# Optimization experiments

Hardware: AMD Instinct MI355X
Metric: run time of the kernel (lower is better)

## Reference

```python
import jax, jax.numpy as jnp
import numpy as np

B, S, F_IN, H, F_OUT, BB = 128, 1024, 128, 256, 128, 256


def setup_inputs() -> dict:
    key = jax.random.key(0)
    ks = jax.random.split(key, 16)
    s_in = 1.0 / np.sqrt(F_IN + H)
    s_bb = 1.0 / np.sqrt(BB)
    s_h = 1.0 / np.sqrt(H)
    return {
        "x": jax.random.normal(ks[0], (B, S, F_IN), dtype=jnp.float32),
        "ts": jax.random.uniform(ks[1], (B, S), dtype=jnp.float32),
        # backbone (depth=1): Linear(F_IN+H -> BB)
        "Wb": jax.random.normal(ks[2], (F_IN + H, BB), dtype=jnp.float32) * s_in,
        "bb": jnp.zeros((BB,), jnp.float32),
        # CfC heads: ff1, ff2, time_a, time_b (BB -> H)
        "Wff1": jax.random.normal(ks[3], (BB, H), dtype=jnp.float32) * s_bb,
        "bff1": jnp.zeros((H,), jnp.float32),
        "Wff2": jax.random.normal(ks[4], (BB, H), dtype=jnp.float32) * s_bb,
        "bff2": jnp.zeros((H,), jnp.float32),
        "Wta": jax.random.normal(ks[5], (BB, H), dtype=jnp.float32) * s_bb,
        "bta": jnp.zeros((H,), jnp.float32),
        "Wtb": jax.random.normal(ks[6], (BB, H), dtype=jnp.float32) * s_bb,
        "btb": jnp.zeros((H,), jnp.float32),
        # output projection Linear(H -> F_OUT)
        "Wout": jax.random.normal(ks[7], (H, F_OUT), dtype=jnp.float32) * s_h,
        "bout": jnp.zeros((F_OUT,), jnp.float32),
    }


def reference(x, ts, Wb, bb, Wff1, bff1, Wff2, bff2, Wta, bta, Wtb, btb, Wout, bout):
    # x: [B,S,F_IN], ts: [B,S] -> out: [B,S,F_OUT]
    batch = x.shape[0]
    hidden = Wff1.shape[1]

    def step(h, inp):
        xt, tt = inp  # xt: [B,F_IN], tt: [B]
        z = jnp.tanh(jnp.concatenate([xt, h], axis=-1) @ Wb + bb)  # backbone [B,BB]
        ff1 = jnp.tanh(z @ Wff1 + bff1)
        ff2 = jnp.tanh(z @ Wff2 + bff2)
        t_a = z @ Wta + bta
        t_b = z @ Wtb + btb
        t_interp = jax.nn.sigmoid(t_a * tt[:, None] + t_b)  # time-dependent gate
        h_new = ff1 * (1.0 - t_interp) + t_interp * ff2
        y = h_new @ Wout + bout
        return h_new, y

    h0 = jnp.zeros((batch, hidden), dtype=x.dtype)
    xs = (jnp.swapaxes(x, 0, 1), jnp.swapaxes(ts, 0, 1))  # time-major for scan
    _, ys = jax.lax.scan(step, h0, xs)  # ys: [S,B,F_OUT]
    return jnp.swapaxes(ys, 0, 1)
```

## Files before the change

kernel.cpp:

```cpp
#include <hip/hip_runtime.h>

#define Bn   128
#define Sn   1024
#define FIN  128
#define Hn   256
#define FOUT 128
#define KBB  384
#define NT1  512

#define NR4 20
#define NL4 1
#define DYN_SMEM ((32 * 256 * 8 + NL4 * 1024 * 8) * 2)

#define NL6 11
#define PF6 12
#define DYN6 ((16 * 256 * 8 + NL6 * 512 * 8) * 2)

#define WB_OFF 0
#define W4_OFF 98304
#define WO_OFF 360448
#define WS_HALVES 393216
#define HBUF_OFF WS_HALVES
#define XC_OFF (HBUF_OFF + (size_t)Bn * Sn * Hn)
#define WS_SPLIT_BYTES ((size_t)(WS_HALVES + (size_t)Bn * Sn * Hn) * 2)
#define WS_FULL_BYTES ((XC_OFF + (size_t)Bn * Sn * Hn) * 2)
#define MBOX_BYTE_OFF WS_FULL_BYTES
#define MBOX_FLOATS ((size_t)Bn * 2 * 2 * 256)
#define CNT_BYTE_OFF (MBOX_BYTE_OFF + MBOX_FLOATS * 4)
#define WS_PAIR_BYTES (CNT_BYTE_OFF + 256 * 4)

typedef _Float16 h2 __attribute__((ext_vector_type(2)));
typedef _Float16 h8 __attribute__((ext_vector_type(8)));

__device__ __forceinline__ float dot2f(h2 a, h2 b, float c) {
#if __has_builtin(__builtin_amdgcn_fdot2)
  return __builtin_amdgcn_fdot2(a, b, c, false);
#else
  return c + (float)a[0] * (float)b[0] + (float)a[1] * (float)b[1];
#endif
}
__device__ __forceinline__ void dot8_4(h8 v, h8 w, float& c0, float& c1, float& c2, float& c3) {
  h2 v0 = {v[0], v[1]}, v1 = {v[2], v[3]}, v2 = {v[4], v[5]}, v3 = {v[6], v[7]};
  h2 w0 = {w[0], w[1]}, w1 = {w[2], w[3]}, w2 = {w[4], w[5]}, w3 = {w[6], w[7]};
  c0 = dot2f(v0, w0, c0); c1 = dot2f(v1, w1, c1);
  c2 = dot2f(v2, w2, c2); c3 = dot2f(v3, w3, c3);
}

__global__ __launch_bounds__(256) void pack_w(
    const float* __restrict__ Wb, const float* __restrict__ W1,
    const float* __restrict__ W2, const float* __restrict__ W3,
    const float* __restrict__ W4, const float* __restrict__ Wo,
    _Float16* __restrict__ ws) {
  int p = blockIdx.x * 256 + threadIdx.x;
  if (p >= WS_HALVES) return;
  float v;
  if (p < W4_OFF) {
    int r = p & 7, j = (p >> 3) & 255;
    int k = ((p >> 11) << 3) | r;
    v = Wb[k * 256 + j];
  } else if (p < WO_OFF) {
    int q = p - W4_OFF;
    int r = q & 7, j = (q >> 3) & 1023;
    int k = ((q >> 13) << 3) | r;
    int jj = j & 255;
    const float* Ws = (j < 256) ? W1 : (j < 512) ? W2 : (j < 768) ? W3 : W4;
    v = Ws[k * 256 + jj];
  } else {
    int q = p - WO_OFF;
    int r = q & 7, j = (q >> 3) & 127;
    int k = ((q >> 10) << 3) | r;
    v = Wo[k * 128 + j];
  }
  ws[p] = (_Float16)v;
}

__global__ void zcnt(unsigned* __restrict__ c) { c[threadIdx.x] = 0; }

__global__ __launch_bounds__(256) void xgemm(
    const float* __restrict__ x, const _Float16* __restrict__ ws,
    _Float16* __restrict__ xc) {
  __shared__ __align__(16) _Float16 sX[64 * 128];
  const int tid = threadIdx.x;
  const size_t r0 = (size_t)blockIdx.x * 64;
  const float* xb = x + r0 * 128;
#pragma unroll
  for (int m = 0; m < 32; ++m)
    sX[m * 256 + tid] = (_Float16)xb[m * 256 + tid];
  const _Float16* gX = ws + WB_OFF + (size_t)tid * 8;
  h8 wx[16];
#pragma unroll
  for (int L = 0; L < 16; ++L) wx[L] = *(const h8*)(gX + (size_t)L * 2048);
  __syncthreads();
  for (int r = 0; r < 64; ++r) {
    float c0 = 0.f, c1 = 0.f, c2 = 0.f, c3 = 0.f;
#pragma unroll
    for (int L = 0; L < 16; ++L) {
      h8 v = *(const h8*)&sX[r * 128 + L * 8];
      dot8_4(v, wx[L], c0, c1, c2, c3);
    }
    xc[(r0 + r) * 256 + tid] = (_Float16)(c0 + c1 + c2 + c3);
  }
}

__global__ __launch_bounds__(NT1) void cfc6(
    const float* __restrict__ ts, const float* __restrict__ bb,
    const float* __restrict__ bf1, const float* __restrict__ bf2,
    const float* __restrict__ bta, const float* __restrict__ btb,
    _Float16* __restrict__ ws, unsigned* __restrict__ cnt,
    float* __restrict__ mbox) {
  __shared__ __align__(16) _Float16 hl[128];
  __shared__ __align__(16) _Float16 zfs[Hn];
  __shared__ float tsb[Sn];
  __shared__ float scrZ[256];
  __shared__ float scrH[384];
  extern __shared__ __align__(16) _Float16 dyn[];
  _Float16* sWbh = dyn;
  _Float16* sW4L = dyn + 16 * 256 * 8;

  const int tid = threadIdx.x;
  const int row = blockIdx.x & 127;
  const int hf  = blockIdx.x >> 7;

  const _Float16* Wb_p = ws + WB_OFF;
  const _Float16* W4_p = ws + W4_OFF;
  _Float16* hbuf = ws + HBUF_OFF;
  const _Float16* xcp = ws + XC_OFF;
  const float* tsrow = ts + (size_t)row * Sn;

  const int jz = tid & 255, kq = tid >> 8;
  const int head = tid >> 7, jj = tid & 127;
  const int jcol = head * 256 + hf * 128 + jj;
  const float bbj = (tid < 256) ? bb[tid] : 0.f;
  const float bH =
      (head == 0 ? bf1 : head == 1 ? bf2 : head == 2 ? bta : btb)[hf * 128 + jj];
  const _Float16* gH = W4_p + (size_t)jcol * 8;

  {
    const h8* src = (const h8*)(Wb_p + (size_t)(16 + hf * 16) * 2048);
    h8* dst = (h8*)sWbh;
    for (int i = tid; i < 16 * 256; i += NT1) dst[i] = src[i];
  }
#pragma unroll
  for (int c = 0; c < NL6; ++c)
    *(h8*)&sW4L[((size_t)c * 512 + tid) * 8] = *(const h8*)(gH + (size_t)c * 8192);
  for (int i = tid; i < Sn; i += NT1) tsb[i] = tsrow[i];
  if (tid < 128) hl[tid] = (_Float16)0.f;

  float* mb_me       = mbox + (size_t)(row * 2 + hf) * 512;
  float* mb_pt       = mbox + (size_t)(row * 2 + (1 - hf)) * 512;
  unsigned* c_me = cnt + row * 2 + hf;
  unsigned* c_pt = cnt + row * 2 + (1 - hf);
  __syncthreads();

  for (unsigned st = 0; st < Sn; ++st) {
    h8 wpf[PF6];
#pragma unroll
    for (int c = 0; c < PF6; ++c)
      wpf[c] = *(const h8*)(gH + (size_t)(NL6 + c) * 8192);
    float xcv = 0.f;
    if (tid < 256) xcv = (float)xcp[((size_t)row * Sn + st) * 256 + tid];

    float a0 = 0.f, a1 = 0.f, a2 = 0.f, a3 = 0.f;
#pragma unroll
    for (int c = kq * 8; c < kq * 8 + 8; ++c) {
      h8 v = *(const h8*)&hl[c * 8];
      h8 w = *(const h8*)&sWbh[((size_t)c * 256 + jz) * 8];
      dot8_4(v, w, a0, a1, a2, a3);
    }
    float zs = a0 + a1 + a2 + a3;
    if (kq) scrZ[jz] = zs;
    __syncthreads();
    float zp = 0.f;
    if (tid < 256) {
      zp = zs + scrZ[tid];
      (void)__hip_atomic_exchange(&mb_me[(st & 1) * 256 + tid], zp,
                                  __ATOMIC_RELAXED, __HIP_MEMORY_SCOPE_AGENT);
    }
    __syncthreads();
    if (tid == 0) {
      __hip_atomic_fetch_add(c_me, 1u, __ATOMIC_RELAXED, __HIP_MEMORY_SCOPE_AGENT);
      while (__hip_atomic_fetch_add(c_pt, 0u, __ATOMIC_RELAXED,
                                    __HIP_MEMORY_SCOPE_AGENT) <= st)
        __builtin_amdgcn_s_sleep(1);
    }
    __syncthreads();
    if (tid < 256) {
      float pz = __hip_atomic_fetch_add(&mb_pt[(st & 1) * 256 + tid], 0.0f,
                                        __ATOMIC_RELAXED, __HIP_MEMORY_SCOPE_AGENT);
      zfs[tid] = (_Float16)tanhf(zp + pz + xcv + bbj);
    }
    __syncthreads();

    float s0 = 0.f, s1 = 0.f, s2 = 0.f, s3 = 0.f;
#pragma unroll 2
    for (int c = NL6 + PF6; c < 32; ++c) {
      h8 v = *(const h8*)&zfs[c * 8];
      h8 w = *(const h8*)(gH + (size_t)c * 8192);
      dot8_4(v, w, s0, s1, s2, s3);
    }
#pragma unroll
    for (int c = 0; c < PF6; ++c) asm volatile("" : "+v"(wpf[c]));
#pragma unroll
    for (int c = 0; c < PF6; ++c) {
      h8 v = *(const h8*)&zfs[(NL6 + c) * 8];
      dot8_4(v, wpf[c], s0, s1, s2, s3);
    }
    float b0 = 0.f, b1 = 0.f, b2 = 0.f, b3 = 0.f;
#pragma unroll
    for (int c = 0; c < NL6; ++c) {
      h8 v = *(const h8*)&zfs[c * 8];
      h8 w = *(const h8*)&sW4L[((size_t)c * 512 + tid) * 8];
      dot8_4(v, w, b0, b1, b2, b3);
    }
    float g = (s0 + b0) + (s1 + b1) + (s2 + b2) + (s3 + b3) + bH;
    if (head) scrH[(head - 1) * 128 + jj] = g;
    __syncthreads();
    if (head == 0) {
      float ff2 = scrH[jj], ta = scrH[128 + jj], tb = scrH[256 + jj];
      float tt = tsb[st];
      float sg = 1.f / (1.f + __expf(-(ta * tt + tb)));
      float hn = tanhf(g) * (1.f - sg) + sg * tanhf(ff2);
      hl[jj] = (_Float16)hn;
      hbuf[((size_t)row * Sn + st) * Hn + hf * 128 + jj] = (_Float16)hn;
    }
    __syncthreads();
  }
}

template <int XC, int INLINE_Y>
__global__ __launch_bounds__(NT1, 2) void cfc5(
    const float* __restrict__ x, const float* __restrict__ ts,
    const float* __restrict__ bb, const float* __restrict__ bf1,
    const float* __restrict__ bf2, const float* __restrict__ bta,
    const float* __restrict__ btb, const float* __restrict__ bo,
    _Float16* __restrict__ ws, float* __restrict__ out) {
  __shared__ __align__(16) _Float16 xh[KBB];
  __shared__ __align__(16) _Float16 zf[Hn];
  __shared__ float tsb[Sn];
  __shared__ float scrZ[256];
  __shared__ float scrH[512];
  extern __shared__ __align__(16) _Float16 dyn[];
  _Float16* sWb  = dyn;
  _Float16* sW4L = dyn + 32 * 256 * 8;

  const int tid = threadIdx.x;
  const int b = blockIdx.x;
  const _Float16* Wb_p = ws + WB_OFF;
  const _Float16* W4_p = ws + W4_OFF;
  const _Float16* Wo_p = ws + WO_OFF;
  _Float16* hbuf = ws + HBUF_OFF;
  const _Float16* xcp = ws + XC_OFF;

  const float* xrow  = x  + (size_t)b * Sn * FIN;
  const float* tsrow = ts + (size_t)b * Sn;
  float*       orow  = out + (size_t)b * Sn * FOUT;

  const int jz = tid & 255, kz = tid >> 8;
  const float bbj = (tid < 256) ? bb[tid] : 0.f;
  const float bHA = (tid < 256) ? bf1[tid] : bf2[tid - 256];
  const float bHB = (tid < 256) ? bta[tid] : btb[tid - 256];
  const int jY = tid & 127, kqY = tid >> 7;
  const float boj = bo[jY];

  if (XC) {
    const h8* src = (const h8*)(Wb_p + (size_t)16 * 2048);
    h8* dst = (h8*)sWb;
    for (int i = tid; i < 8192; i += NT1) dst[i] = src[i];
  }
  {
    const h8* src = (const h8*)(W4_p + (size_t)NR4 * 8192);
    h8* dst = (h8*)sW4L;
    for (int i = tid; i < NL4 * 1024; i += NT1) dst[i] = src[i];
  }
  for (int i = tid; i < Sn; i += NT1) tsb[i] = tsrow[i];
  if (tid < 128) ((unsigned*)xh)[64 + tid] = 0;
  if (!XC && tid < 64) {
    float2 xv = *(const float2*)(xrow + 2 * tid);
    h2 p; p[0] = (_Float16)xv.x; p[1] = (_Float16)xv.y;
    *(h2*)&xh[2 * tid] = p;
  }

  const _Float16* gA = W4_p + (size_t)tid * 8;
  const _Float16* gB = W4_p + (size_t)(tid + 512) * 8;
  h8 wA[NR4], wBv[NR4];
#pragma unroll
  for (int c = 0; c < NR4; ++c) {
    wA[c]  = *(const h8*)(gA + (size_t)c * 8192);
    wBv[c] = *(const h8*)(gB + (size_t)c * 8192);
  }
#pragma unroll
  for (int c = 0; c < NR4; ++c) {
    asm volatile("" : "+v"(wA[c]));
    asm volatile("" : "+v"(wBv[c]));
  }
  __syncthreads();

  for (int st = 0; st < Sn; ++st) {
    float xcv = 0.f;
    if (XC && tid < 256)
      xcv = (float)xcp[((size_t)b * Sn + st) * 256 + tid];
    float2 xv; xv.x = 0.f; xv.y = 0.f;
    if (!XC && tid >= 448 && st + 1 < Sn)
      xv = *(const float2*)(xrow + (size_t)(st + 1) * FIN + 2 * (tid - 448));

    float a0 = 0.f, a1 = 0.f, a2 = 0.f, a3 = 0.f;
    if (XC) {
#pragma unroll 4
      for (int c = 0; c < 16; ++c) {
        int kc = kz * 16 + c;
        h8 v = *(const h8*)&xh[128 + kc * 8];
        h8 w = *(const h8*)&sWb[((size_t)kc * 256 + jz) * 8];
        dot8_4(v, w, a0, a1, a2, a3);
      }
    } else {
      const _Float16* gZ = Wb_p + ((size_t)(kz * 24) * 256 + jz) * 8;
#pragma unroll 4
      for (int c = 0; c < 24; ++c) {
        h8 v = *(const h8*)&xh[(kz * 24 + c) * 8];
        h8 w = *(const h8*)(gZ + (size_t)c * 2048);
        dot8_4(v, w, a0, a1, a2, a3);
      }
    }
    float zs = a0 + a1 + a2 + a3;
    if (kz) scrZ[jz] = zs;
    __syncthreads();
    if (tid < 256) {
      float zp = zs + scrZ[tid] + bbj;
      if (XC) zp += xcv;
      zf[tid] = (_Float16)tanhf(zp);
    }
    if (!XC && tid >= 448 && st + 1 < Sn) {
      h2 p; p[0] = (_Float16)xv.x; p[1] = (_Float16)xv.y;
      *(h2*)&xh[2 * (tid - 448)] = p;
    }
    __syncthreads();

    float hA0 = 0.f, hA1 = 0.f, hA2 = 0.f, hA3 = 0.f;
    float hB0 = 0.f, hB1 = 0.f, hB2 = 0.f, hB3 = 0.f;
#pragma unroll 2
    for (int c = NR4 + NL4; c < 32; ++c) {
      h8 v  = *(const h8*)&zf[c * 8];
      h8 wa = *(const h8*)(gA + (size_t)c * 8192);
      h8 wb = *(const h8*)(gB + (size_t)c * 8192);
      dot8_4(v, wa, hA0, hA1, hA2, hA3);
      dot8_4(v, wb, hB0, hB1, hB2, hB3);
    }
#pragma unroll
    for (int c = 0; c < NR4; ++c) {
      h8 v = *(const h8*)&zf[c * 8];
      dot8_4(v, wA[c],  hA0, hA1, hA2, hA3);
      dot8_4(v, wBv[c], hB0, hB1, hB2, hB3);
    }
#pragma unroll
    for (int l = 0; l < NL4; ++l) {
      h8 v  = *(const h8*)&zf[(NR4 + l) * 8];
      h8 wa = *(const h8*)&sW4L[((size_t)l * 1024 + tid) * 8];
      h8 wb = *(const h8*)&sW4L[((size_t)l * 1024 + tid + 512) * 8];
      dot8_4(v, wa, hA0, hA1, hA2, hA3);
      dot8_4(v, wb, hB0, hB1, hB2, hB3);
    }
    float gAv = hA0 + hA1 + hA2 + hA3 + bHA;
    float gBv = hB0 + hB1 + hB2 + hB3 + bHB;
    if (tid >= 256) {
      scrH[tid - 256]       = gAv;
      scrH[256 + tid - 256] = gBv;
    }
    __syncthreads();
    if (tid < 256) {
      float ff2v = scrH[tid], tbv = scrH[256 + tid];
      float tt = tsb[st];
      float sg = 1.f / (1.f + __expf(-(gBv * tt + tbv)));
      float hn = tanhf(gAv) * (1.f - sg) + sg * tanhf(ff2v);
      xh[128 + tid] = (_Float16)hn;
      if (!INLINE_Y)
        hbuf[((size_t)b * Sn + st) * Hn + tid] = (_Float16)hn;
    }
    __syncthreads();

    if (INLINE_Y) {
      const _Float16* gY = Wo_p + ((size_t)(kqY * 8) * 128 + jY) * 8;
      float y0 = 0.f, y1 = 0.f, y2 = 0.f, y3 = 0.f;
#pragma unroll
      for (int c = 0; c < 8; ++c) {
        h8 v = *(const h8*)&xh[128 + (kqY * 8 + c) * 8];
        h8 w = *(const h8*)(gY + (size_t)c * 1024);
        dot8_4(v, w, y0, y1, y2, y3);
      }
      float ysv = y0 + y1 + y2 + y3;
      if (kqY) scrH[(kqY - 1) * 128 + jY] = ysv;
      __syncthreads();
      if (kqY == 0) {
        float y = ysv + boj + scrH[jY] + scrH[128 + jY] + scrH[256 + jY];
        orow[(size_t)st * FOUT + jY] = y;
      }
    }
  }
}

#define SMEMY (65536 + 4096)
extern "C" __global__ __launch_bounds__(256, 4)
void ygemm(const _Float16* __restrict__ ws, const float* __restrict__ bo,
           float* __restrict__ out) {
  extern __shared__ char ysm[];
  _Float16* sWo = (_Float16*)ysm;
  _Float16* sH  = (_Float16*)(ysm + 65536);
  const int tid = threadIdx.x;
  { const uint4* g = (const uint4*)(ws + WO_OFF);
    uint4* l = (uint4*)sWo;
#pragma unroll
    for (int i = 0; i < 16; ++i) l[tid + 256 * i] = g[tid + 256 * i]; }
  const _Float16* hb = ws + HBUF_OFF;
  const int row0 = blockIdx.x * 256;
  const int j = tid & 127, rh = tid >> 7;
  const float boj = bo[j];
  for (int it = 0; it < 32; ++it) {
    const int rbase = row0 + it * 8;
    __syncthreads();
    ((uint4*)sH)[tid] = ((const uint4*)(hb + (size_t)rbase * 256))[tid];
    __syncthreads();
#pragma unroll
    for (int rr = rh; rr < 8; rr += 2) {
      float y0 = 0.f, y1 = 0.f, y2 = 0.f, y3 = 0.f;
#pragma unroll 4
      for (int c = 0; c < 32; ++c) {
        h8 v = *(const h8*)&sH[rr * 256 + c * 8];
        h8 w = *(const h8*)&sWo[((size_t)c * 128 + j) * 8];
        dot8_4(v, w, y0, y1, y2, y3);
      }
      out[(size_t)(rbase + rr) * 128 + j] = y0 + y1 + y2 + y3 + boj;
    }
  }
}

extern "C" void kernel_launch(void* const* d_in, const int* in_sizes, int n_in,
                              void* d_out, int out_size, void* d_ws, size_t ws_size,
                              hipStream_t stream) {
  const float* x   = (const float*)d_in[0];
  const float* ts  = (const float*)d_in[1];
  const float* Wb  = (const float*)d_in[2];
  const float* bb  = (const float*)d_in[3];
  const float* W1  = (const float*)d_in[4];
  const float* bf1 = (const float*)d_in[5];
  const float* W2  = (const float*)d_in[6];
  const float* bf2 = (const float*)d_in[7];
  const float* W3  = (const float*)d_in[8];
  const float* bta = (const float*)d_in[9];
  const float* W4  = (const float*)d_in[10];
  const float* btb = (const float*)d_in[11];
  const float* Wo  = (const float*)d_in[12];
  const float* bo  = (const float*)d_in[13];
  float* out = (float*)d_out;
  _Float16* ws = (_Float16*)d_ws;

  pack_w<<<WS_HALVES / 256, 256, 0, stream>>>(Wb, W1, W2, W3, W4, Wo, ws);

  if (ws_size >= WS_PAIR_BYTES) {
    zcnt<<<1, 256, 0, stream>>>((unsigned*)((char*)d_ws + CNT_BYTE_OFF));
    xgemm<<<(Bn * Sn) / 64, 256, 0, stream>>>(x, ws, ws + XC_OFF);
    hipFuncSetAttribute((const void*)cfc6,
                        hipFuncAttributeMaxDynamicSharedMemorySize, DYN6);
    cfc6<<<2 * Bn, NT1, DYN6, stream>>>(
        ts, bb, bf1, bf2, bta, btb, ws,
        (unsigned*)((char*)d_ws + CNT_BYTE_OFF),
        (float*)((char*)d_ws + MBOX_BYTE_OFF));
    hipFuncSetAttribute((const void*)ygemm,
                        hipFuncAttributeMaxDynamicSharedMemorySize, SMEMY);
    ygemm<<<(Bn * Sn) / 256, 256, SMEMY, stream>>>(ws, bo, out);
  } else if (ws_size >= WS_FULL_BYTES) {
    xgemm<<<(Bn * Sn) / 64, 256, 0, stream>>>(x, ws, ws + XC_OFF);
    hipFuncSetAttribute((const void*)(cfc5<1, 0>),
                        hipFuncAttributeMaxDynamicSharedMemorySize, DYN_SMEM);
    cfc5<1, 0><<<Bn, NT1, DYN_SMEM, stream>>>(x, ts, bb, bf1, bf2, bta, btb, bo, ws, out);
    hipFuncSetAttribute((const void*)ygemm,
                        hipFuncAttributeMaxDynamicSharedMemorySize, SMEMY);
    ygemm<<<(Bn * Sn) / 256, 256, SMEMY, stream>>>(ws, bo, out);
  } else if (ws_size >= WS_SPLIT_BYTES) {
    hipFuncSetAttribute((const void*)(cfc5<0, 0>),
                        hipFuncAttributeMaxDynamicSharedMemorySize, DYN_SMEM);
    cfc5<0, 0><<<Bn, NT1, DYN_SMEM, stream>>>(x, ts, bb, bf1, bf2, bta, btb, bo, ws, out);
    hipFuncSetAttribute((const void*)ygemm,
                        hipFuncAttributeMaxDynamicSharedMemorySize, SMEMY);
    ygemm<<<(Bn * Sn) / 256, 256, SMEMY, stream>>>(ws, bo, out);
  } else {
    hipFuncSetAttribute((const void*)(cfc5<0, 1>),
                        hipFuncAttributeMaxDynamicSharedMemorySize, DYN_SMEM);
    cfc5<0, 1><<<Bn, NT1, DYN_SMEM, stream>>>(x, ts, bb, bf1, bf2, bta, btb, bo, ws, out);
  }
}
```

Measured before the change: 4.796 ms.

## Replace counter-based pair handshake with step-tagged 64-bit mailbox words

Each of the two blocks that share a batch row now writes its partial backbone sums as 64-bit words, with the step index in the upper half. The partner spins on each word until the tag matches. This removes the separate counter increment, the single-thread spin loop and two block-wide barriers per timestep from the serial recurrence. The weight prefetch depth also grows from 12 to 16 chunks, which adds register pressure, and the whole mailbox must now be zeroed before launch.

Measured after the change: 4.239 ms. 11.6% less time.

```diff
diff --git a/kernel.cpp b/kernel.cpp
--- a/kernel.cpp
+++ b/kernel.cpp
@@ -13,7 +13,7 @@
 #define DYN_SMEM ((32 * 256 * 8 + NL4 * 1024 * 8) * 2)
 
 #define NL6 11
-#define PF6 12
+#define PF6 16
 #define DYN6 ((16 * 256 * 8 + NL6 * 512 * 8) * 2)
 
 #define WB_OFF 0
@@ -25,9 +25,8 @@
 #define WS_SPLIT_BYTES ((size_t)(WS_HALVES + (size_t)Bn * Sn * Hn) * 2)
 #define WS_FULL_BYTES ((XC_OFF + (size_t)Bn * Sn * Hn) * 2)
 #define MBOX_BYTE_OFF WS_FULL_BYTES
-#define MBOX_FLOATS ((size_t)Bn * 2 * 2 * 256)
-#define CNT_BYTE_OFF (MBOX_BYTE_OFF + MBOX_FLOATS * 4)
-#define WS_PAIR_BYTES (CNT_BYTE_OFF + 256 * 4)
+#define MBOX_WORDS ((size_t)Bn * 2 * 2 * 256)
+#define WS_PAIR_BYTES (MBOX_BYTE_OFF + MBOX_WORDS * 8)
 
 typedef _Float16 h2 __attribute__((ext_vector_type(2)));
 typedef _Float16 h8 __attribute__((ext_vector_type(8)));
@@ -74,7 +73,9 @@
   ws[p] = (_Float16)v;
 }
 
-__global__ void zcnt(unsigned* __restrict__ c) { c[threadIdx.x] = 0; }
+__global__ void zmbox(unsigned long long* __restrict__ m) {
+  m[(size_t)blockIdx.x * 256 + threadIdx.x] = 0ull;
+}
 
 __global__ __launch_bounds__(256) void xgemm(
     const float* __restrict__ x, const _Float16* __restrict__ ws,
@@ -106,8 +107,7 @@
     const float* __restrict__ ts, const float* __restrict__ bb,
     const float* __restrict__ bf1, const float* __restrict__ bf2,
     const float* __restrict__ bta, const float* __restrict__ btb,
-    _Float16* __restrict__ ws, unsigned* __restrict__ cnt,
-    float* __restrict__ mbox) {
+    _Float16* __restrict__ ws, unsigned long long* __restrict__ mbox) {
   __shared__ __align__(16) _Float16 hl[128];
   __shared__ __align__(16) _Float16 zfs[Hn];
   __shared__ float tsb[Sn];
@@ -146,10 +146,8 @@
   for (int i = tid; i < Sn; i += NT1) tsb[i] = tsrow[i];
   if (tid < 128) hl[tid] = (_Float16)0.f;
 
-  float* mb_me       = mbox + (size_t)(row * 2 + hf) * 512;
-  float* mb_pt       = mbox + (size_t)(row * 2 + (1 - hf)) * 512;
-  unsigned* c_me = cnt + row * 2 + hf;
-  unsigned* c_pt = cnt + row * 2 + (1 - hf);
+  unsigned long long* mb_me = mbox + (size_t)(row * 2 + hf) * 512;
+  unsigned long long* mb_pt = mbox + (size_t)(row * 2 + (1 - hf)) * 512;
   __syncthreads();
 
   for (unsigned st = 0; st < Sn; ++st) {
@@ -170,23 +168,18 @@
     float zs = a0 + a1 + a2 + a3;
     if (kq) scrZ[jz] = zs;
     __syncthreads();
-    float zp = 0.f;
     if (tid < 256) {
-      zp = zs + scrZ[tid];
-      (void)__hip_atomic_exchange(&mb_me[(st & 1) * 256 + tid], zp,
+      float zp = zs + scrZ[tid];
+      unsigned long long w =
+          ((unsigned long long)(st + 1) << 32) | (unsigned long long)__float_as_uint(zp);
+      (void)__hip_atomic_exchange(&mb_me[(st & 1) * 256 + tid], w,
                                   __ATOMIC_RELAXED, __HIP_MEMORY_SCOPE_AGENT);
-    }
-    __syncthreads();
-    if (tid == 0) {
-      __hip_atomic_fetch_add(c_me, 1u, __ATOMIC_RELAXED, __HIP_MEMORY_SCOPE_AGENT);
-      while (__hip_atomic_fetch_add(c_pt, 0u, __ATOMIC_RELAXED,
-                                    __HIP_MEMORY_SCOPE_AGENT) <= st)
-        __builtin_amdgcn_s_sleep(1);
-    }
-    __syncthreads();
-    if (tid < 256) {
-      float pz = __hip_atomic_fetch_add(&mb_pt[(st & 1) * 256 + tid], 0.0f,
-                                        __ATOMIC_RELAXED, __HIP_MEMORY_SCOPE_AGENT);
+      unsigned long long r;
+      do {
+        r = __hip_atomic_fetch_add(&mb_pt[(st & 1) * 256 + tid], 0ull,
+                                   __ATOMIC_RELAXED, __HIP_MEMORY_SCOPE_AGENT);
+      } while ((unsigned)(r >> 32) != st + 1);
+      float pz = __uint_as_float((unsigned)r);
       zfs[tid] = (_Float16)tanhf(zp + pz + xcv + bbj);
     }
     __syncthreads();
@@ -455,14 +448,14 @@
   pack_w<<<WS_HALVES / 256, 256, 0, stream>>>(Wb, W1, W2, W3, W4, Wo, ws);
 
   if (ws_size >= WS_PAIR_BYTES) {
-    zcnt<<<1, 256, 0, stream>>>((unsigned*)((char*)d_ws + CNT_BYTE_OFF));
+    zmbox<<<MBOX_WORDS / 256, 256, 0, stream>>>(
+        (unsigned long long*)((char*)d_ws + MBOX_BYTE_OFF));
     xgemm<<<(Bn * Sn) / 64, 256, 0, stream>>>(x, ws, ws + XC_OFF);
     hipFuncSetAttribute((const void*)cfc6,
                         hipFuncAttributeMaxDynamicSharedMemorySize, DYN6);
     cfc6<<<2 * Bn, NT1, DYN6, stream>>>(
         ts, bb, bf1, bf2, bta, btb, ws,
-        (unsigned*)((char*)d_ws + CNT_BYTE_OFF),
-        (float*)((char*)d_ws + MBOX_BYTE_OFF));
+        (unsigned long long*)((char*)d_ws + MBOX_BYTE_OFF));
     hipFuncSetAttribute((const void*)ygemm,
                         hipFuncAttributeMaxDynamicSharedMemorySize, SMEMY);
     ygemm<<<(Bn * Sn) / 256, 256, SMEMY, stream>>>(ws, bo, out);
```
